# Kernel tuning notes

Hardware: AMD Instinct MI355X
Metric: run time of the kernel (lower is better)

The kernel has to match this reference:

```python
import jax, jax.numpy as jnp
import numpy as np

NUM_EXPERTS = 8
DIM = 1024
HIDDEN = 2048
N_TOKENS = 8192  # rows of x, includes padding beyond sum(num_tokens_per_expert)


def setup_inputs() -> dict:
    key = jax.random.key(0)
    k_x, k_w1, k_w2, k_w3 = jax.random.split(key, 4)
    x = jax.random.normal(k_x, (N_TOKENS, DIM), dtype=jnp.float32)
    # trunc_normal(std=0.02)-like init; w2 is zeros in torch init but we use
    w1 = jax.random.normal(k_w1, (NUM_EXPERTS, HIDDEN, DIM), dtype=jnp.float32) * 0.02
    w2 = jax.random.normal(k_w2, (NUM_EXPERTS, DIM, HIDDEN), dtype=jnp.float32) * 0.02
    w3 = jax.random.normal(k_w3, (NUM_EXPERTS, HIDDEN, DIM), dtype=jnp.float32) * 0.02
    # routed token counts per expert; sum <= N_TOKENS, remainder is padding
    num_tokens_per_expert = jnp.array([995, 1000, 980, 1010, 970, 1020, 990, 1005], dtype=jnp.int64)
    return {"x": x, "num_tokens_per_expert": num_tokens_per_expert,
            "w1": w1, "w2": w2, "w3": w3}


def reference(x, num_tokens_per_expert, w1, w2, w3):
    # Mirrors torch _run_experts_for_loop with act='silu'. The torch code calls
    # .tolist() on the counts (shapes are data-dependent), so we likewise treat
    # the per-expert counts as static host values.
    counts = np.asarray(num_tokens_per_expert).astype(np.int64)
    offsets = np.concatenate([np.zeros(1, np.int64), np.cumsum(counts)])
    total = int(offsets[-1])
    num_experts = w1.shape[0]
    out_splits = []
    for e in range(num_experts):
        xe = x[int(offsets[e]):int(offsets[e + 1])]            # [n_e, dim]
        gate = jax.nn.silu(xe @ w1[e].T)                       # [n_e, hidden]
        h = gate * (xe @ w3[e].T)                              # SwiGLU
        out_splits.append(h @ w2[e].T)                         # [n_e, dim]
    out = jnp.concatenate(out_splits, axis=0)
    num_padding = x.shape[0] - total
    if num_padding > 0:
        out = jnp.concatenate([out, jnp.zeros((num_padding, out.shape[-1]), out.dtype)], axis=0)
    return out
```

## Files before the change

kernel.cpp:

```cpp
#include <hip/hip_runtime.h>

#define NEXP 8
#define DIM  1024
#define HID  2048
#define NTOK 8192

#define BM 128
#define BN 128
#define BK 32

typedef short s16x8 __attribute__((ext_vector_type(8)));
typedef float f32x4 __attribute__((ext_vector_type(4)));
typedef unsigned short u16;

__device__ __forceinline__ u16 f2bf(float f) {
  unsigned int u = __builtin_bit_cast(unsigned int, f);
  u += 0x7FFFu + ((u >> 16) & 1u);
  return (u16)(u >> 16);
}

__device__ __forceinline__ ushort4 cvt4(float4 a) {
  ushort4 r; r.x = f2bf(a.x); r.y = f2bf(a.y); r.z = f2bf(a.z); r.w = f2bf(a.w); return r;
}

__device__ __forceinline__ s16x8 pk8(float4 a, float4 b) {
  union { unsigned u[4]; s16x8 v; } P;
  asm("v_cvt_pk_bf16_f32 %0, %1, %2" : "=v"(P.u[0]) : "v"(a.x), "v"(a.y));
  asm("v_cvt_pk_bf16_f32 %0, %1, %2" : "=v"(P.u[1]) : "v"(a.z), "v"(a.w));
  asm("v_cvt_pk_bf16_f32 %0, %1, %2" : "=v"(P.u[2]) : "v"(b.x), "v"(b.y));
  asm("v_cvt_pk_bf16_f32 %0, %1, %2" : "=v"(P.u[3]) : "v"(b.z), "v"(b.w));
  return P.v;
}

__device__ __forceinline__ void gload16(const u16* g, u16* l) {
  __builtin_amdgcn_global_load_lds((const __attribute__((address_space(1))) void*)g,
                                   (__attribute__((address_space(3))) void*)l, 16, 0, 0);
}

__device__ __forceinline__ void BAR() {
  asm volatile("s_waitcnt lgkmcnt(0)" ::: "memory");
  __builtin_amdgcn_s_barrier();
  asm volatile("" ::: "memory");
}

__device__ __forceinline__ bool find_tile(const int* __restrict__ cnts, int rt,
                                          int& e_out, int& row0, int& cnt_out, long long& off_out) {
  long long off = 0; int cum = 0;
  #pragma unroll
  for (int e = 0; e < NEXP; ++e) {
    int c = cnts[e];
    int nt = (c + BM - 1) / BM;
    if (rt < cum + nt) { e_out = e; row0 = (rt - cum) * BM; cnt_out = c; off_out = off; return true; }
    cum += nt; off += c;
  }
  return false;
}

__global__ __launch_bounds__(256) void cvt_x(const float* __restrict__ in,
                                             u16* __restrict__ out, int n4) {
  const int i = blockIdx.x * 256 + threadIdx.x;
  if (i < n4) ((ushort4*)out)[i] = cvt4(((const float4*)in)[i]);
}

#define XSTR 68
__global__ __launch_bounds__(512, 4) void gemm1_hyb(
    const u16* __restrict__ xb, const int* __restrict__ cnts,
    const float* __restrict__ w1, const float* __restrict__ w3,
    u16* __restrict__ hbuf)
{
  int e, row0, cnt; long long off;
  if (!find_tile(cnts, blockIdx.y, e, row0, cnt, off)) return;
  const int ct = blockIdx.x;

  __shared__ __align__(16) float smem_f[4 * 64 * XSTR];
  u16* lds = (u16*)smem_f;

  const int t    = threadIdx.x;
  const int lane = t & 63;
  const int wid  = t >> 6;
  const int mat  = wid >> 2;
  const int sw   = wid & 3;
  const int wr = sw >> 1, wc = sw & 1;
  const int lr = lane & 15;
  const int lk = (((lane >> 4) ^ ((lr >> 1) & 3)) << 3);

  const int q    = lane >> 2;
  const int cf   = (lane & 3) ^ ((q >> 1) & 3);
  const int srow = wid * 16 + q;

  const u16*   xr  = xb + (size_t)(off + row0) * DIM;
  const float* w1t = w1 + ((size_t)e * HID + (size_t)ct * BN) * DIM;
  const float* w3t = w3 + ((size_t)e * HID + (size_t)ct * BN) * DIM;
  const size_t gaoff = (size_t)srow * DIM + cf * 8;

  f32x4 acc[4][4];
  const f32x4 zf = {0.f, 0.f, 0.f, 0.f};
  #pragma unroll
  for (int i = 0; i < 4; ++i)
    #pragma unroll
    for (int j = 0; j < 4; ++j) acc[i][j] = zf;

  float4 S[4];
  auto ADMA = [&](int k0, int ab) {
    gload16(&xr[gaoff + k0], lds + ab * 4096 + wid * 512);
  };
  auto WLOAD = [&](int k0) {
    const size_t go = gaoff + k0;
    S[0] = *(const float4*)&w1t[go]; S[1] = *(const float4*)&w1t[go + 4];
    S[2] = *(const float4*)&w3t[go]; S[3] = *(const float4*)&w3t[go + 4];
  };
  auto WRITE_W = [&](int wb) {
    u16* base = lds + 12288 + wb * 8192 + wid * 512 + lane * 8;
    *(s16x8*)(base)        = pk8(S[0], S[1]);
    *(s16x8*)(base + 4096) = pk8(S[2], S[3]);
  };
  auto COMPUTE = [&](int ab, int wb) {
    const u16* Asb = lds + ab * 4096;
    const u16* Bsb = lds + 12288 + wb * 8192 + mat * 4096;
    s16x8 af[4], bf[4];
    #pragma unroll
    for (int fm = 0; fm < 4; ++fm)
      af[fm] = *(const s16x8*)&Asb[(wr * 64 + fm * 16 + lr) * BK + lk];
    #pragma unroll
    for (int fn = 0; fn < 4; ++fn)
      bf[fn] = *(const s16x8*)&Bsb[(wc * 64 + fn * 16 + lr) * BK + lk];
    __builtin_amdgcn_s_setprio(1);
    #pragma unroll
    for (int fm = 0; fm < 4; ++fm)
      #pragma unroll
      for (int fn = 0; fn < 4; ++fn)
        acc[fm][fn] = __builtin_amdgcn_mfma_f32_16x16x32_bf16(af[fm], bf[fn], acc[fm][fn], 0, 0, 0);
    __builtin_amdgcn_s_setprio(0);
  };

  const int NT = DIM / BK;
  ADMA(0, 0);
  ADMA(BK, 1);
  WLOAD(0);
  WRITE_W(0);
  WLOAD(BK);
  BAR();
  for (int kt = 0; kt < NT; ++kt) {
    if (kt + 2 < NT) ADMA((kt + 2) * BK, (kt + 2) % 3);
    COMPUTE(kt % 3, kt & 1);
    if (kt + 1 < NT) {
      WRITE_W((kt + 1) & 1);
      if (kt + 2 < NT) WLOAD((kt + 2) * BK);
    }
    BAR();
  }

  __syncthreads();
  if (mat) {
    float* up = smem_f + sw * (64 * XSTR);
    #pragma unroll
    for (int fm = 0; fm < 4; ++fm)
      #pragma unroll
      for (int fn = 0; fn < 4; ++fn)
        #pragma unroll
        for (int j = 0; j < 4; ++j)
          up[(fm * 16 + ((lane >> 4) << 2) + j) * XSTR + fn * 16 + lr] = acc[fm][fn][j];
  }
  __syncthreads();
  if (!mat) {
    const float* up = smem_f + sw * (64 * XSTR);
    #pragma unroll
    for (int fm = 0; fm < 4; ++fm)
      #pragma unroll
      for (int fn = 0; fn < 4; ++fn) {
        const int col = ct * BN + wc * 64 + fn * 16 + lr;
        #pragma unroll
        for (int j = 0; j < 4; ++j) {
          const int r = wr * 64 + fm * 16 + ((lane >> 4) << 2) + j;
          if (row0 + r < cnt) {
            const float gv = acc[fm][fn][j];
            const float uv = up[(fm * 16 + ((lane >> 4) << 2) + j) * XSTR + fn * 16 + lr];
            const float hv = (gv / (1.f + __expf(-gv))) * uv;
            hbuf[(size_t)(off + row0 + r) * HID + col] = f2bf(hv);
          }
        }
      }
  }
}

__global__ __launch_bounds__(256, 4) void gemm2_hyb(
    const u16* __restrict__ hbuf, const int* __restrict__ cnts,
    const float* __restrict__ w2, float* __restrict__ out)
{
  int e, row0, cnt; long long off;
  if (!find_tile(cnts, blockIdx.y, e, row0, cnt, off)) return;
  const int ct = blockIdx.x;

  __shared__ __align__(16) u16 lds[20480];

  const int t    = threadIdx.x;
  const int lane = t & 63;
  const int wid  = t >> 6;
  const int wr = wid >> 1, wc = wid & 1;
  const int lr = lane & 15;
  const int lk = (((lane >> 4) ^ ((lr >> 1) & 3)) << 3);

  const int q  = lane >> 2;
  const int cf = (lane & 3) ^ ((q >> 1) & 3);

  const u16*   ar  = hbuf + (size_t)(off + row0) * HID;
  const float* w2t = w2 + ((size_t)e * DIM + (size_t)ct * BN) * HID;
  const size_t g0 = (size_t)(wid * 32 + q) * HID + cf * 8;
  const size_t g1 = (size_t)(wid * 32 + 16 + q) * HID + cf * 8;

  f32x4 acc[4][4];
  const f32x4 zf = {0.f, 0.f, 0.f, 0.f};
  #pragma unroll
  for (int i = 0; i < 4; ++i)
    #pragma unroll
    for (int j = 0; j < 4; ++j) acc[i][j] = zf;

  float4 S[4];
  auto ADMA = [&](int k0, int ab) {
    u16* base = lds + ab * 4096;
    gload16(&ar[g0 + k0], base + (wid * 2 + 0) * 512);
    gload16(&ar[g1 + k0], base + (wid * 2 + 1) * 512);
  };
  auto WLOAD = [&](int k0) {
    S[0] = *(const float4*)&w2t[g0 + k0]; S[1] = *(const float4*)&w2t[g0 + k0 + 4];
    S[2] = *(const float4*)&w2t[g1 + k0]; S[3] = *(const float4*)&w2t[g1 + k0 + 4];
  };
  auto WRITE_W = [&](int wb) {
    u16* base = lds + 12288 + wb * 4096;
    *(s16x8*)(base + (wid * 2 + 0) * 512 + lane * 8) = pk8(S[0], S[1]);
    *(s16x8*)(base + (wid * 2 + 1) * 512 + lane * 8) = pk8(S[2], S[3]);
  };
  auto COMPUTE = [&](int ab, int wb) {
    const u16* Asb = lds + ab * 4096;
    const u16* Bsb = lds + 12288 + wb * 4096;
    s16x8 af[4], bf[4];
    #pragma unroll
    for (int fm = 0; fm < 4; ++fm)
      af[fm] = *(const s16x8*)&Asb[(wr * 64 + fm * 16 + lr) * BK + lk];
    #pragma unroll
    for (int fn = 0; fn < 4; ++fn)
      bf[fn] = *(const s16x8*)&Bsb[(wc * 64 + fn * 16 + lr) * BK + lk];
    #pragma unroll
    for (int fm = 0; fm < 4; ++fm)
      #pragma unroll
      for (int fn = 0; fn < 4; ++fn)
        acc[fm][fn] = __builtin_amdgcn_mfma_f32_16x16x32_bf16(af[fm], bf[fn], acc[fm][fn], 0, 0, 0);
  };

  const int NT = HID / BK;
  ADMA(0, 0);
  ADMA(BK, 1);
  WLOAD(0);
  WRITE_W(0);
  WLOAD(BK);
  BAR();
  for (int kt = 0; kt < NT; ++kt) {
    if (kt + 2 < NT) ADMA((kt + 2) * BK, (kt + 2) % 3);
    COMPUTE(kt % 3, kt & 1);
    if (kt + 1 < NT) {
      WRITE_W((kt + 1) & 1);
      if (kt + 2 < NT) WLOAD((kt + 2) * BK);
    }
    BAR();
  }

  #pragma unroll
  for (int fm = 0; fm < 4; ++fm)
    #pragma unroll
    for (int fn = 0; fn < 4; ++fn) {
      const int col = ct * BN + wc * 64 + fn * 16 + lr;
      #pragma unroll
      for (int j = 0; j < 4; ++j) {
        const int r = wr * 64 + fm * 16 + ((lane >> 4) << 2) + j;
        if (row0 + r < cnt)
          out[(size_t)(off + row0 + r) * DIM + col] = acc[fm][fn][j];
      }
    }
}

__global__ void zero_pad_kernel(const int* __restrict__ cnts, float* __restrict__ out)
{
  int total = 0;
  #pragma unroll
  for (int e = 0; e < NEXP; ++e) total += cnts[e];
  const int row = blockIdx.x;
  if (row < total) return;
  float4* p = (float4*)(out + (size_t)row * DIM);
  p[threadIdx.x] = make_float4(0.f, 0.f, 0.f, 0.f);
}

extern "C" void kernel_launch(void* const* d_in, const int* in_sizes, int n_in,
                              void* d_out, int out_size, void* d_ws, size_t ws_size,
                              hipStream_t stream) {
  const float* x    = (const float*)d_in[0];
  const int*   cnts = (const int*)d_in[1];
  const float* w1   = (const float*)d_in[2];
  const float* w2   = (const float*)d_in[3];
  const float* w3   = (const float*)d_in[4];
  float*       out  = (float*)d_out;

  u16* hbuf = (u16*)d_ws;
  u16* xb   = hbuf + (size_t)NTOK * HID;

  const int X4 = NTOK * DIM / 4;
  cvt_x<<<dim3(X4 / 256), dim3(256), 0, stream>>>(x, xb, X4);
  gemm1_hyb<<<dim3(HID / BN, 72), dim3(512), 0, stream>>>(xb, cnts, w1, w3, hbuf);
  gemm2_hyb<<<dim3(DIM / BN, 72), dim3(256), 0, stream>>>(hbuf, cnts, w2, out);
  zero_pad_kernel<<<dim3(NTOK), dim3(256), 0, stream>>>(cnts, out);
}
```

Baseline: 202.6 us.

## Deepen weight prefetch with double register sets and explicit vmcnt waits

```diff
diff --git a/kernel.cpp b/kernel.cpp
--- a/kernel.cpp
+++ b/kernel.cpp
@@ -37,7 +37,17 @@
                                    (__attribute__((address_space(3))) void*)l, 16, 0, 0);
 }
 
-__device__ __forceinline__ void BAR() {
+__device__ __forceinline__ void vwait(int n) {
+  switch (n) {
+    case 0:  asm volatile("s_waitcnt vmcnt(0)"  ::: "memory"); break;
+    case 5:  asm volatile("s_waitcnt vmcnt(5)"  ::: "memory"); break;
+    case 6:  asm volatile("s_waitcnt vmcnt(6)"  ::: "memory"); break;
+    case 9:  asm volatile("s_waitcnt vmcnt(9)"  ::: "memory"); break;
+    case 10: asm volatile("s_waitcnt vmcnt(10)" ::: "memory"); break;
+    default: asm volatile("s_waitcnt vmcnt(0)"  ::: "memory"); break;
+  }
+}
+__device__ __forceinline__ void BARX() {
   asm volatile("s_waitcnt lgkmcnt(0)" ::: "memory");
   __builtin_amdgcn_s_barrier();
   asm volatile("" ::: "memory");
@@ -100,23 +110,24 @@
     #pragma unroll
     for (int j = 0; j < 4; ++j) acc[i][j] = zf;
 
-  float4 S[4];
+  f32x4 SA[4], SB[4];
+
   auto ADMA = [&](int k0, int ab) {
     gload16(&xr[gaoff + k0], lds + ab * 4096 + wid * 512);
   };
-  auto WLOAD = [&](int k0) {
+  auto WLOAD = [&](int k0, f32x4 (&S)[4]) {
     const size_t go = gaoff + k0;
-    S[0] = *(const float4*)&w1t[go]; S[1] = *(const float4*)&w1t[go + 4];
-    S[2] = *(const float4*)&w3t[go]; S[3] = *(const float4*)&w3t[go + 4];
-  };
-  auto WRITE_W = [&](int wb) {
-    u16* base = lds + 12288 + wb * 8192 + wid * 512 + lane * 8;
-    *(s16x8*)(base)        = pk8(S[0], S[1]);
-    *(s16x8*)(base + 4096) = pk8(S[2], S[3]);
+    S[0] = *(const f32x4*)&w1t[go]; S[1] = *(const f32x4*)&w1t[go + 4];
+    S[2] = *(const f32x4*)&w3t[go]; S[3] = *(const f32x4*)&w3t[go + 4];
+  };
+  auto WRITE_W = [&](int wb, f32x4 (&S)[4]) {
+    u16* base = lds + 16384 + wb * 8192 + wid * 512 + lane * 8;
+    *(s16x8*)(base)        = pk8(*(float4*)&S[0], *(float4*)&S[1]);
+    *(s16x8*)(base + 4096) = pk8(*(float4*)&S[2], *(float4*)&S[3]);
   };
   auto COMPUTE = [&](int ab, int wb) {
     const u16* Asb = lds + ab * 4096;
-    const u16* Bsb = lds + 12288 + wb * 8192 + mat * 4096;
+    const u16* Bsb = lds + 16384 + wb * 8192 + mat * 4096;
     s16x8 af[4], bf[4];
     #pragma unroll
     for (int fm = 0; fm < 4; ++fm)
@@ -132,23 +143,29 @@
         acc[fm][fn] = __builtin_amdgcn_mfma_f32_16x16x32_bf16(af[fm], bf[fn], acc[fm][fn], 0, 0, 0);
     __builtin_amdgcn_s_setprio(0);
   };
+  auto BODY = [&](int kt, f32x4 (&S)[4], bool doA, bool doL, bool doW, int vn) {
+    if (doA) ADMA((kt + 2) * BK, (kt + 2) & 3);
+    COMPUTE(kt & 3, kt & 1);
+    if (doW) WRITE_W((kt + 1) & 1, S);
+    if (doL) WLOAD((kt + 3) * BK, S);
+    vwait(vn);
+    BARX();
+  };
 
   const int NT = DIM / BK;
-  ADMA(0, 0);
-  ADMA(BK, 1);
-  WLOAD(0);
-  WRITE_W(0);
-  WLOAD(BK);
-  BAR();
-  for (int kt = 0; kt < NT; ++kt) {
-    if (kt + 2 < NT) ADMA((kt + 2) * BK, (kt + 2) % 3);
-    COMPUTE(kt % 3, kt & 1);
-    if (kt + 1 < NT) {
-      WRITE_W((kt + 1) & 1);
-      if (kt + 2 < NT) WLOAD((kt + 2) * BK);
-    }
-    BAR();
-  }
+  ADMA(0, 0); ADMA(BK, 1);
+  WLOAD(0, SA); WLOAD(BK, SB);
+  WRITE_W(0, SA);
+  WLOAD(2 * BK, SA);
+  BARX();
+  for (int kt = 0; kt + 4 < NT; kt += 2) {
+    BODY(kt,     SB, true, true, true, 9);
+    BODY(kt + 1, SA, true, true, true, 9);
+  }
+  BODY(NT - 4, SB, true,  true,  true, 9);
+  BODY(NT - 3, SA, true,  false, true, 5);
+  BODY(NT - 2, SB, false, false, true, 0);
+  COMPUTE((NT - 1) & 3, (NT - 1) & 1);
 
   __syncthreads();
   if (mat) {
@@ -191,7 +208,7 @@
   if (!find_tile(cnts, blockIdx.y, e, row0, cnt, off)) return;
   const int ct = blockIdx.x;
 
-  __shared__ __align__(16) u16 lds[20480];
+  __shared__ __align__(16) u16 lds[24576];
 
   const int t    = threadIdx.x;
   const int lane = t & 63;
@@ -215,24 +232,25 @@
     #pragma unroll
     for (int j = 0; j < 4; ++j) acc[i][j] = zf;
 
-  float4 S[4];
+  f32x4 SA[4], SB[4];
+
   auto ADMA = [&](int k0, int ab) {
     u16* base = lds + ab * 4096;
     gload16(&ar[g0 + k0], base + (wid * 2 + 0) * 512);
     gload16(&ar[g1 + k0], base + (wid * 2 + 1) * 512);
   };
-  auto WLOAD = [&](int k0) {
-    S[0] = *(const float4*)&w2t[g0 + k0]; S[1] = *(const float4*)&w2t[g0 + k0 + 4];
-    S[2] = *(const float4*)&w2t[g1 + k0]; S[3] = *(const float4*)&w2t[g1 + k0 + 4];
-  };
-  auto WRITE_W = [&](int wb) {
-    u16* base = lds + 12288 + wb * 4096;
-    *(s16x8*)(base + (wid * 2 + 0) * 512 + lane * 8) = pk8(S[0], S[1]);
-    *(s16x8*)(base + (wid * 2 + 1) * 512 + lane * 8) = pk8(S[2], S[3]);
+  auto WLOAD = [&](int k0, f32x4 (&S)[4]) {
+    S[0] = *(const f32x4*)&w2t[g0 + k0]; S[1] = *(const f32x4*)&w2t[g0 + k0 + 4];
+    S[2] = *(const f32x4*)&w2t[g1 + k0]; S[3] = *(const f32x4*)&w2t[g1 + k0 + 4];
+  };
+  auto WRITE_W = [&](int wb, f32x4 (&S)[4]) {
+    u16* base = lds + 16384 + wb * 4096;
+    *(s16x8*)(base + (wid * 2 + 0) * 512 + lane * 8) = pk8(*(float4*)&S[0], *(float4*)&S[1]);
+    *(s16x8*)(base + (wid * 2 + 1) * 512 + lane * 8) = pk8(*(float4*)&S[2], *(float4*)&S[3]);
   };
   auto COMPUTE = [&](int ab, int wb) {
     const u16* Asb = lds + ab * 4096;
-    const u16* Bsb = lds + 12288 + wb * 4096;
+    const u16* Bsb = lds + 16384 + wb * 4096;
     s16x8 af[4], bf[4];
     #pragma unroll
     for (int fm = 0; fm < 4; ++fm)
@@ -246,23 +264,29 @@
       for (int fn = 0; fn < 4; ++fn)
         acc[fm][fn] = __builtin_amdgcn_mfma_f32_16x16x32_bf16(af[fm], bf[fn], acc[fm][fn], 0, 0, 0);
   };
+  auto BODY = [&](int kt, f32x4 (&S)[4], bool doA, bool doL, bool doW, int vn) {
+    if (doA) ADMA((kt + 2) * BK, (kt + 2) & 3);
+    COMPUTE(kt & 3, kt & 1);
+    if (doW) WRITE_W((kt + 1) & 1, S);
+    if (doL) WLOAD((kt + 3) * BK, S);
+    vwait(vn);
+    BARX();
+  };
 
   const int NT = HID / BK;
-  ADMA(0, 0);
-  ADMA(BK, 1);
-  WLOAD(0);
-  WRITE_W(0);
-  WLOAD(BK);
-  BAR();
-  for (int kt = 0; kt < NT; ++kt) {
-    if (kt + 2 < NT) ADMA((kt + 2) * BK, (kt + 2) % 3);
-    COMPUTE(kt % 3, kt & 1);
-    if (kt + 1 < NT) {
-      WRITE_W((kt + 1) & 1);
-      if (kt + 2 < NT) WLOAD((kt + 2) * BK);
-    }
-    BAR();
-  }
+  ADMA(0, 0); ADMA(BK, 1);
+  WLOAD(0, SA); WLOAD(BK, SB);
+  WRITE_W(0, SA);
+  WLOAD(2 * BK, SA);
+  BARX();
+  for (int kt = 0; kt + 4 < NT; kt += 2) {
+    BODY(kt,     SB, true, true, true, 10);
+    BODY(kt + 1, SA, true, true, true, 10);
+  }
+  BODY(NT - 4, SB, true,  true,  true, 10);
+  BODY(NT - 3, SA, true,  false, true, 6);
+  BODY(NT - 2, SB, false, false, true, 0);
+  COMPUTE((NT - 1) & 3, (NT - 1) & 1);
 
   #pragma unroll
   for (int fm = 0; fm < 4; ++fm)
```

After: 389.1 us. 1.92x slower.
